# Kernel tuning notes

Hardware: AMD Instinct MI355X
Metric: run time of the kernel (lower is better)

Reference implementation:

```python
import jax, jax.numpy as jnp
import numpy as np

H = 256  # hidden dim, hard-coded in the torch module
DROP_P = 0.25


def setup_inputs() -> dict:
    key = jax.random.key(0)
    ks = jax.random.split(key, 8)
    B, T, D, C = 512, 512, 128, 1000
    x = jax.random.normal(ks[0], (B, T, D), dtype=jnp.float32)
    W_ih = jax.random.normal(ks[1], (3 * H, D), dtype=jnp.float32) * (1.0 / np.sqrt(H))
    W_hh = jax.random.normal(ks[2], (3 * H, H), dtype=jnp.float32) * (1.0 / np.sqrt(H))
    b_ih = jax.random.normal(ks[3], (3 * H,), dtype=jnp.float32) * 0.01
    b_hh = jax.random.normal(ks[4], (3 * H,), dtype=jnp.float32) * 0.01
    W_out = jax.random.normal(ks[5], (C, H), dtype=jnp.float32) * (1.0 / np.sqrt(H))
    b_out = jax.random.normal(ks[6], (C,), dtype=jnp.float32) * 0.01
    # inverted dropout masks per timestep: [T, B, H]
    keep = jax.random.bernoulli(ks[7], 1.0 - DROP_P, (T, B, H))
    drop_mask = keep.astype(jnp.float32) / (1.0 - DROP_P)
    return {"x": x, "W_ih": W_ih, "W_hh": W_hh, "b_ih": b_ih, "b_hh": b_hh,
            "W_out": W_out, "b_out": b_out, "drop_mask": drop_mask}


def _gru_scan(x_tbd, drop_mask, W_ih, W_hh, b_ih, b_hh):
    B = x_tbd.shape[1]
    h0 = jnp.zeros((B, H), dtype=x_tbd.dtype)

    def step(h, inp):
        x_t, m_t = inp
        gi = x_t @ W_ih.T + b_ih        # [B, 3H]
        gh = h @ W_hh.T + b_hh          # [B, 3H]
        i_r, i_z, i_n = gi[:, :H], gi[:, H:2 * H], gi[:, 2 * H:]
        h_r, h_z, h_n = gh[:, :H], gh[:, H:2 * H], gh[:, 2 * H:]
        r = jax.nn.sigmoid(i_r + h_r)
        z = jax.nn.sigmoid(i_z + h_z)
        n = jnp.tanh(i_n + r * h_n)
        h_new = (1.0 - z) * n + z * h
        h_new = h_new * m_t             # dropout per timestep
        return h_new, None

    h_final, _ = jax.lax.scan(step, h0, (x_tbd, drop_mask))
    return h_final


def reference(x, W_ih, W_hh, b_ih, b_hh, W_out, b_out, drop_mask):
    # x: [B, T, D] -> time-major [T, B, D] for scan
    x_tbd = jnp.transpose(x, (1, 0, 2))
    h = _gru_scan(x_tbd, drop_mask, W_ih, W_hh, b_ih, b_hh)
    return h @ W_out.T + b_out          # [B, num_classes]
```

## Files before the change

kernel.cpp:

```cpp
#include <hip/hip_runtime.h>
#include <stdint.h>

#define T_STEPS 512
#define BATCH   512
#define DIN     128
#define HID     256
#define NCLS    1000

typedef unsigned int u32;
typedef unsigned long long u64;
typedef __attribute__((ext_vector_type(8))) short  short8;
typedef __attribute__((ext_vector_type(4))) short  short4v;
typedef __attribute__((ext_vector_type(4))) float  f32x4;

__device__ __forceinline__ short f2bf(float f){
  u32 u = __float_as_uint(f);
  u32 r = (u + 0x7FFFu + ((u >> 16) & 1u)) >> 16;
  return (short)r;
}
__device__ __forceinline__ float bf2f(unsigned short s){
  return __uint_as_float(((u32)s) << 16);
}
__device__ __forceinline__ short8 cvt8(f32x4 a, f32x4 b){
  short8 v;
  v[0]=f2bf(a[0]); v[1]=f2bf(a[1]); v[2]=f2bf(a[2]); v[3]=f2bf(a[3]);
  v[4]=f2bf(b[0]); v[5]=f2bf(b[1]); v[6]=f2bf(b[2]); v[7]=f2bf(b[3]);
  return v;
}
__device__ __forceinline__ void gload_lds16(const void* g, void* l){
  __builtin_amdgcn_global_load_lds(
      (const __attribute__((address_space(1))) unsigned int*)g,
      (__attribute__((address_space(3))) unsigned int*)l, 16, 0, 0);
}

__global__ __launch_bounds__(256) void pack_weights(
    const float* __restrict__ Wih, const float* __restrict__ Whh,
    short* __restrict__ PIH, short* __restrict__ PHH)
{
  int idx = blockIdx.x * 256 + threadIdx.x;
  if (idx >= 48*768) return;
  const float* src; short* dst;
  if (idx < 16*768){
    int kb = idx / 768, j = idx - kb*768;
    src = Wih + (size_t)j*DIN + kb*8;
    dst = PIH + (size_t)idx*8;
  } else {
    int i2 = idx - 16*768;
    int kb = i2 / 768, j = i2 - kb*768;
    src = Whh + (size_t)j*HID + kb*8;
    dst = PHH + (size_t)i2*8;
  }
  short8 v;
  #pragma unroll
  for (int e=0;e<8;e++) v[e] = f2bf(src[e]);
  *(short8*)dst = v;
}

__global__ __launch_bounds__(256) void mask_bits(
    const float* __restrict__ mask, unsigned char* __restrict__ MBo)
{
  int idx = blockIdx.x*256 + threadIdx.x;
  int t = idx >> 14, rem = idx & 16383, bb = rem >> 5, ub = rem & 31;
  const float* mp = mask + ((size_t)t*BATCH + bb)*HID + ub*8;
  u32 byte = 0;
  #pragma unroll
  for (int e=0;e<8;e++) byte |= (mp[e] > 0.5f ? 1u : 0u) << e;
  MBo[((size_t)t*64 + (bb>>3))*256 + (bb&7)*32 + ub] = (unsigned char)byte;
}

__global__ __launch_bounds__(512, 1) void gi_gemm(
    const float* __restrict__ x, const float* __restrict__ b_ih,
    const float* __restrict__ b_hh, const short* __restrict__ PIH,
    short* __restrict__ GIbf, float* __restrict__ GIn)
{
  __shared__ __align__(16) short XT[64*136];
  const int tid = threadIdx.x;
  const int gb  = blockIdx.x >> 6;
  const int tc  = blockIdx.x & 63;
  const int tp0 = tc*4;
  const int w = tid>>6, l = tid&63, c = l&15, g4 = l>>4;

  short8 bfr[6][4]; float bj[6];
  #pragma unroll
  for (int q=0;q<6;q++){
    const int j = (w*6+q)*16 + c;
    #pragma unroll
    for (int kt=0;kt<4;kt++)
      bfr[q][kt] = *(const short8*)(PIH + ((size_t)(kt*4+g4)*768 + j)*8);
    bj[q] = b_ih[j] + (j < 512 ? b_hh[j] : 0.f);
  }

  {
    const int row = tid>>3, cc = (tid&7)*16;
    const int r = row&7, tpl = row>>4, tt = (row>>3)&1;
    const int bb = gb*8 + r;
    const int t  = (tp0+tpl)*2 + tt;
    const float* src = x + ((size_t)bb*T_STEPS + t)*DIN + cc;
    f32x4 a0 = *(const f32x4*)src,     a1 = *(const f32x4*)(src+4);
    f32x4 a2 = *(const f32x4*)(src+8), a3 = *(const f32x4*)(src+12);
    *(short8*)&XT[row*136 + cc]     = cvt8(a0,a1);
    *(short8*)&XT[row*136 + cc + 8] = cvt8(a2,a3);
  }
  __syncthreads();

  const f32x4 z4 = {0.f,0.f,0.f,0.f};
  #pragma unroll
  for (int mt=0; mt<4; ++mt){
    f32x4 acc[6];
    #pragma unroll
    for (int q=0;q<6;q++) acc[q] = z4;
    #pragma unroll
    for (int kt=0;kt<4;kt++){
      short8 af = *(const short8*)&XT[(mt*16+c)*136 + kt*32 + g4*8];
      #pragma unroll
      for (int q=0;q<6;q++)
        acc[q] = __builtin_amdgcn_mfma_f32_16x16x32_bf16(af, bfr[q][kt], acc[q], 0,0,0);
    }
    const int tp = tp0 + mt;
    const size_t base16 = ((size_t)gb*256 + tp)*16;
    #pragma unroll
    for (int q=0;q<6;q++){
      const int j = (w*6+q)*16 + c;
      if (j < 512){
        #pragma unroll
        for (int i=0;i<4;i++)
          GIbf[(base16 + g4*4+i)*512 + j] = f2bf(acc[q][i] + bj[q]);
      } else {
        #pragma unroll
        for (int i=0;i<4;i++)
          GIn[(base16 + g4*4+i)*256 + (j-512)] = acc[q][i] + bj[q];
      }
    }
  }
}

__global__ __launch_bounds__(512, 1) void gru_scan(
    const float* __restrict__ b_hh, const unsigned char* __restrict__ MB,
    const short* __restrict__ PHH, const short* __restrict__ GIbf,
    const float* __restrict__ GIn, float* __restrict__ HFIN)
{
  __shared__ __align__(16) short Ah[16*264];
  __shared__ __align__(16) float Gs[8*776];
  __shared__ __align__(16) short GiRZ[2][8*512];
  __shared__ __align__(16) float GiN [2][8*256];

  const int tid = threadIdx.x;
  const int gb  = blockIdx.x;
  const int w = tid>>6, l = tid&63, c = l&15, g4 = l>>4;

  short8 whf[6][8];
  #pragma unroll
  for (int q=0;q<6;q++){
    const int j = (w*6+q)*16 + c;
    #pragma unroll
    for (int kt=0;kt<8;kt++)
      whf[q][kt] = *(const short8*)(PHH + ((size_t)(kt*4+g4)*768 + j)*8);
  }

  const int b  = tid>>6;
  const int u4 = (tid&63)*4;
  const f32x4 bhn4 = *(const f32x4*)(b_hh + 512 + u4);
  const int mboff = b*32 + ((tid&63)>>1);
  const int mshift = ((tid&63)&1) << 2;

  for (int i=tid; i<16*264; i+=512) Ah[i] = 0;

  const char* srz = (const char*)GIbf + (size_t)gb*256*16*512*2;
  const char* sn  = (const char*)GIn  + (size_t)gb*256*16*256*4;

  {
    gload_lds16(srz + (size_t)0*8192 + w*1024 + l*16, (char*)&GiRZ[0][w*512]);
    gload_lds16(sn  + (size_t)0*8192 + w*1024 + l*16, (char*)&GiN [0][w*256]);
  }
  u32 mbcur = MB[(size_t)gb*256 + mboff];
  float hreg[4] = {0.f,0.f,0.f,0.f};
  asm volatile("s_waitcnt vmcnt(0)" ::: "memory");
  __syncthreads();

  const int ar_off = c*264;
  const f32x4 z4 = {0.f,0.f,0.f,0.f};

  for (int t=0; t<T_STEPS; ++t){
    const int buf = t & 1;
    u32 mbnext = 0;
    if (t < T_STEPS-1){
      gload_lds16(srz + (size_t)(t+1)*8192 + w*1024 + l*16, (char*)&GiRZ[buf^1][w*512]);
      gload_lds16(sn  + (size_t)(t+1)*8192 + w*1024 + l*16, (char*)&GiN [buf^1][w*256]);
      mbnext = MB[((size_t)(t+1)*64 + gb)*256 + mboff];
    }
    f32x4 acc[6];
    #pragma unroll
    for (int q=0;q<6;q++) acc[q] = z4;
    #pragma unroll
    for (int kt=0;kt<8;kt++){
      short8 af = *(const short8*)&Ah[ar_off + kt*32 + g4*8];
      #pragma unroll
      for (int q=0;q<6;q++)
        acc[q] = __builtin_amdgcn_mfma_f32_16x16x32_bf16(af, whf[q][kt], acc[q], 0,0,0);
    }
    if (g4 < 2){
      #pragma unroll
      for (int q=0;q<6;q++){
        const int j = (w*6+q)*16 + c;
        #pragma unroll
        for (int i=0;i<4;i++)
          Gs[(g4*4+i)*776 + j] = acc[q][i];
      }
    }
    asm volatile("s_waitcnt lgkmcnt(0)" ::: "memory");
    __builtin_amdgcn_sched_barrier(0);
    __builtin_amdgcn_s_barrier();
    __builtin_amdgcn_sched_barrier(0);
    {
      f32x4 gr = *(const f32x4*)&Gs[b*776       + u4];
      f32x4 gz = *(const f32x4*)&Gs[b*776 + 256 + u4];
      f32x4 gn = *(const f32x4*)&Gs[b*776 + 512 + u4];
      short4v sr = *(const short4v*)&GiRZ[buf][b*512       + u4];
      short4v sz = *(const short4v*)&GiRZ[buf][b*512 + 256 + u4];
      f32x4 gin = *(const f32x4*)&GiN[buf][b*256 + u4];
      short hb0,hb1,hb2,hb3;
      #pragma unroll
      for (int e=0;e<4;e++){
        float r_ = 1.f/(1.f + __expf(-(gr[e] + bf2f((unsigned short)sr[e]))));
        float z_ = 1.f/(1.f + __expf(-(gz[e] + bf2f((unsigned short)sz[e]))));
        float e2 = __expf(2.f*(gin[e] + r_*(gn[e] + bhn4[e])));
        float n_ = 1.f - 2.f/(e2 + 1.f);
        float mv = ((mbcur >> (mshift + e)) & 1u) ? 1.3333334f : 0.f;
        hreg[e] = ((1.f - z_)*n_ + z_*hreg[e]) * mv;
      }
      hb0=f2bf(hreg[0]); hb1=f2bf(hreg[1]); hb2=f2bf(hreg[2]); hb3=f2bf(hreg[3]);
      short4v hv; hv[0]=hb0; hv[1]=hb1; hv[2]=hb2; hv[3]=hb3;
      *(short4v*)&Ah[b*264 + u4] = hv;
    }
    mbcur = mbnext;
    asm volatile("s_waitcnt vmcnt(0)" ::: "memory");
    __syncthreads();
  }

  f32x4 hv; hv[0]=hreg[0]; hv[1]=hreg[1]; hv[2]=hreg[2]; hv[3]=hreg[3];
  *(f32x4*)&HFIN[((size_t)(gb*8 + b))*HID + u4] = hv;
}

__global__ __launch_bounds__(256) void out_gemm(
    const float* __restrict__ Hf, const float* __restrict__ Wout,
    const float* __restrict__ bout, float* __restrict__ out)
{
  __shared__ __align__(16) float hl[16*256];
  const int bb0 = (blockIdx.x >> 4) * 16;
  const int cc0 = (blockIdx.x & 15) * 64;
  for (int i=threadIdx.x; i<16*256; i+=256) hl[i] = Hf[(size_t)bb0*HID + i];
  __syncthreads();
  const int cc = cc0 + (threadIdx.x & 63);
  const int br = threadIdx.x >> 6;
  if (cc >= NCLS) return;
  const f32x4* wr = (const f32x4*)(Wout + (size_t)cc*HID);
  float a0=0.f, a1=0.f, a2=0.f, a3=0.f;
  #pragma unroll 8
  for (int k4=0;k4<64;k4++){
    f32x4 wv = wr[k4];
    #pragma unroll
    for (int e=0;e<4;e++){
      float we = wv[e]; int k = k4*4+e;
      a0 += hl[(br   )*256+k]*we;
      a1 += hl[(br+ 4)*256+k]*we;
      a2 += hl[(br+ 8)*256+k]*we;
      a3 += hl[(br+12)*256+k]*we;
    }
  }
  float bo = bout[cc];
  out[(size_t)(bb0+br   )*NCLS + cc] = a0 + bo;
  out[(size_t)(bb0+br+ 4)*NCLS + cc] = a1 + bo;
  out[(size_t)(bb0+br+ 8)*NCLS + cc] = a2 + bo;
  out[(size_t)(bb0+br+12)*NCLS + cc] = a3 + bo;
}

extern "C" void kernel_launch(void* const* d_in, const int* in_sizes, int n_in,
                              void* d_out, int out_size, void* d_ws, size_t ws_size,
                              hipStream_t stream) {
  const float* x     = (const float*)d_in[0];
  const float* W_ih  = (const float*)d_in[1];
  const float* W_hh  = (const float*)d_in[2];
  const float* b_ih  = (const float*)d_in[3];
  const float* b_hh  = (const float*)d_in[4];
  const float* W_out = (const float*)d_in[5];
  const float* b_out = (const float*)d_in[6];
  const float* dmask = (const float*)d_in[7];

  if (ws_size < 546373632ull) return;
  short* PIH  = (short*)d_ws;
  short* PHH  = (short*)((char*)d_ws + 196608);
  float* HFIN = (float*)((char*)d_ws + 589824);
  unsigned char* MBp = (unsigned char*)d_ws + 1114112;
  short* GIbf = (short*)((char*)d_ws + 9502720);
  float* GIn  = (float*)((char*)d_ws + 277938176);

  pack_weights<<<144, 256, 0, stream>>>(W_ih, W_hh, PIH, PHH);
  mask_bits<<<32768, 256, 0, stream>>>(dmask, MBp);
  gi_gemm<<<4096, 512, 0, stream>>>(x, b_ih, b_hh, PIH, GIbf, GIn);
  gru_scan<<<64, 512, 0, stream>>>(b_hh, MBp, PHH, GIbf, GIn, HFIN);
  out_gemm<<<512, 256, 0, stream>>>(HFIN, W_out, b_out, (float*)d_out);
}
```

Measured before the change: 1.787 ms.

## Stage GI outputs through LDS for coalesced stores; register-prefetch scan inputs

The input-projection GEMM now writes its results into shared-memory tiles and then stores them to global memory as contiguous 16-byte vectors, replacing scattered 2- and 4-byte stores. The recurrent scan drops the asynchronous global-to-LDS double buffer and instead prefetches the next timestep's gate inputs and mask bits into registers. Each step copies these into a single LDS buffer, and the loop is unrolled by two so the register buffers alternate. Launch bounds for the scan are raised to allow two blocks per CU. In exchange the scan adds a second barrier per step and higher register pressure, which could cause spills.

```diff
diff --git a/kernel.cpp b/kernel.cpp
--- a/kernel.cpp
+++ b/kernel.cpp
@@ -26,11 +26,6 @@
   v[0]=f2bf(a[0]); v[1]=f2bf(a[1]); v[2]=f2bf(a[2]); v[3]=f2bf(a[3]);
   v[4]=f2bf(b[0]); v[5]=f2bf(b[1]); v[6]=f2bf(b[2]); v[7]=f2bf(b[3]);
   return v;
-}
-__device__ __forceinline__ void gload_lds16(const void* g, void* l){
-  __builtin_amdgcn_global_load_lds(
-      (const __attribute__((address_space(1))) unsigned int*)g,
-      (__attribute__((address_space(3))) unsigned int*)l, 16, 0, 0);
 }
 
 __global__ __launch_bounds__(256) void pack_weights(
@@ -74,6 +69,8 @@
     short* __restrict__ GIbf, float* __restrict__ GIn)
 {
   __shared__ __align__(16) short XT[64*136];
+  __shared__ __align__(16) short ORZ[16*520];
+  __shared__ __align__(16) float ON [16*264];
   const int tid = threadIdx.x;
   const int gb  = blockIdx.x >> 6;
   const int tc  = blockIdx.x & 63;
@@ -104,7 +101,7 @@
   __syncthreads();
 
   const f32x4 z4 = {0.f,0.f,0.f,0.f};
-  #pragma unroll
+  #pragma unroll 1
   for (int mt=0; mt<4; ++mt){
     f32x4 acc[6];
     #pragma unroll
@@ -116,33 +113,55 @@
       for (int q=0;q<6;q++)
         acc[q] = __builtin_amdgcn_mfma_f32_16x16x32_bf16(af, bfr[q][kt], acc[q], 0,0,0);
     }
-    const int tp = tp0 + mt;
-    const size_t base16 = ((size_t)gb*256 + tp)*16;
     #pragma unroll
     for (int q=0;q<6;q++){
       const int j = (w*6+q)*16 + c;
-      if (j < 512){
-        #pragma unroll
-        for (int i=0;i<4;i++)
-          GIbf[(base16 + g4*4+i)*512 + j] = f2bf(acc[q][i] + bj[q]);
-      } else {
-        #pragma unroll
-        for (int i=0;i<4;i++)
-          GIn[(base16 + g4*4+i)*256 + (j-512)] = acc[q][i] + bj[q];
+      #pragma unroll
+      for (int i=0;i<4;i++){
+        const int r16 = g4*4+i;
+        const float v = acc[q][i] + bj[q];
+        if (j < 512) ORZ[r16*520 + j] = f2bf(v);
+        else         ON [r16*264 + (j-512)] = v;
       }
     }
-  }
-}
-
-__global__ __launch_bounds__(512, 1) void gru_scan(
+    __syncthreads();
+    {
+      const size_t gbase = (size_t)gb*2097152;
+      #pragma unroll
+      for (int pass=0; pass<2; ++pass){
+        const int chunk = pass*512 + tid;
+        const int tt  = chunk >> 9;
+        const int rem = chunk & 511;
+        const int row = rem >> 6, c16 = rem & 63;
+        short8 vv = *(const short8*)&ORZ[(tt*8+row)*520 + c16*8];
+        const int t = (tp0+mt)*2 + tt;
+        *(short8*)(GIbf + gbase + (size_t)t*4096 + rem*8) = vv;
+      }
+      const size_t nbase = (size_t)gb*1048576;
+      #pragma unroll
+      for (int pass=0; pass<2; ++pass){
+        const int chunk = pass*512 + tid;
+        const int tt  = chunk >> 9;
+        const int rem = chunk & 511;
+        const int row = rem >> 6, c4 = rem & 63;
+        f32x4 vv = *(const f32x4*)&ON[(tt*8+row)*264 + c4*4];
+        const int t = (tp0+mt)*2 + tt;
+        *(f32x4*)(GIn + nbase + (size_t)t*2048 + rem*4) = vv;
+      }
+    }
+    __syncthreads();
+  }
+}
+
+__global__ __launch_bounds__(512, 2) void gru_scan(
     const float* __restrict__ b_hh, const unsigned char* __restrict__ MB,
     const short* __restrict__ PHH, const short* __restrict__ GIbf,
     const float* __restrict__ GIn, float* __restrict__ HFIN)
 {
   __shared__ __align__(16) short Ah[16*264];
   __shared__ __align__(16) float Gs[8*776];
-  __shared__ __align__(16) short GiRZ[2][8*512];
-  __shared__ __align__(16) float GiN [2][8*256];
+  __shared__ __align__(16) short GiRZs[8*512];
+  __shared__ __align__(16) float GiNs [8*256];
 
   const int tid = threadIdx.x;
   const int gb  = blockIdx.x;
@@ -165,77 +184,85 @@
 
   for (int i=tid; i<16*264; i+=512) Ah[i] = 0;
 
-  const char* srz = (const char*)GIbf + (size_t)gb*256*16*512*2;
-  const char* sn  = (const char*)GIn  + (size_t)gb*256*16*256*4;
-
-  {
-    gload_lds16(srz + (size_t)0*8192 + w*1024 + l*16, (char*)&GiRZ[0][w*512]);
-    gload_lds16(sn  + (size_t)0*8192 + w*1024 + l*16, (char*)&GiN [0][w*256]);
-  }
-  u32 mbcur = MB[(size_t)gb*256 + mboff];
+  const char* srz = (const char*)GIbf + (size_t)gb*4194304;
+  const char* sn  = (const char*)GIn  + (size_t)gb*4194304;
+  const int gioff = w*1024 + l*16;
+  const int ar_off = c*264;
+  const int gbase = (g4*4)*776 + w*96 + c;
+
+  asm volatile("" ::: "memory");
+
+  short8 rzA = *(const short8*)(srz + gioff);
+  f32x4  nA  = *(const f32x4 *)(sn  + gioff);
+  u32    mkA = MB[(size_t)gb*256 + mboff];
+  short8 rzB; f32x4 nB; u32 mkB;
   float hreg[4] = {0.f,0.f,0.f,0.f};
-  asm volatile("s_waitcnt vmcnt(0)" ::: "memory");
   __syncthreads();
 
-  const int ar_off = c*264;
   const f32x4 z4 = {0.f,0.f,0.f,0.f};
 
-  for (int t=0; t<T_STEPS; ++t){
-    const int buf = t & 1;
-    u32 mbnext = 0;
-    if (t < T_STEPS-1){
-      gload_lds16(srz + (size_t)(t+1)*8192 + w*1024 + l*16, (char*)&GiRZ[buf^1][w*512]);
-      gload_lds16(sn  + (size_t)(t+1)*8192 + w*1024 + l*16, (char*)&GiN [buf^1][w*256]);
-      mbnext = MB[((size_t)(t+1)*64 + gb)*256 + mboff];
-    }
-    f32x4 acc[6];
-    #pragma unroll
-    for (int q=0;q<6;q++) acc[q] = z4;
-    #pragma unroll
-    for (int kt=0;kt<8;kt++){
-      short8 af = *(const short8*)&Ah[ar_off + kt*32 + g4*8];
-      #pragma unroll
-      for (int q=0;q<6;q++)
-        acc[q] = __builtin_amdgcn_mfma_f32_16x16x32_bf16(af, whf[q][kt], acc[q], 0,0,0);
-    }
-    if (g4 < 2){
-      #pragma unroll
-      for (int q=0;q<6;q++){
-        const int j = (w*6+q)*16 + c;
-        #pragma unroll
-        for (int i=0;i<4;i++)
-          Gs[(g4*4+i)*776 + j] = acc[q][i];
-      }
-    }
-    asm volatile("s_waitcnt lgkmcnt(0)" ::: "memory");
-    __builtin_amdgcn_sched_barrier(0);
-    __builtin_amdgcn_s_barrier();
-    __builtin_amdgcn_sched_barrier(0);
-    {
-      f32x4 gr = *(const f32x4*)&Gs[b*776       + u4];
-      f32x4 gz = *(const f32x4*)&Gs[b*776 + 256 + u4];
-      f32x4 gn = *(const f32x4*)&Gs[b*776 + 512 + u4];
-      short4v sr = *(const short4v*)&GiRZ[buf][b*512       + u4];
-      short4v sz = *(const short4v*)&GiRZ[buf][b*512 + 256 + u4];
-      f32x4 gin = *(const f32x4*)&GiN[buf][b*256 + u4];
-      short hb0,hb1,hb2,hb3;
-      #pragma unroll
-      for (int e=0;e<4;e++){
-        float r_ = 1.f/(1.f + __expf(-(gr[e] + bf2f((unsigned short)sr[e]))));
-        float z_ = 1.f/(1.f + __expf(-(gz[e] + bf2f((unsigned short)sz[e]))));
-        float e2 = __expf(2.f*(gin[e] + r_*(gn[e] + bhn4[e])));
-        float n_ = 1.f - 2.f/(e2 + 1.f);
-        float mv = ((mbcur >> (mshift + e)) & 1u) ? 1.3333334f : 0.f;
-        hreg[e] = ((1.f - z_)*n_ + z_*hreg[e]) * mv;
-      }
-      hb0=f2bf(hreg[0]); hb1=f2bf(hreg[1]); hb2=f2bf(hreg[2]); hb3=f2bf(hreg[3]);
-      short4v hv; hv[0]=hb0; hv[1]=hb1; hv[2]=hb2; hv[3]=hb3;
-      *(short4v*)&Ah[b*264 + u4] = hv;
-    }
-    mbcur = mbnext;
-    asm volatile("s_waitcnt vmcnt(0)" ::: "memory");
-    __syncthreads();
-  }
+#define STEP(T, RZC, NC, MC, RZN, NN, MN) {                                    \
+  const int tn = ((T) < T_STEPS-1) ? (T)+1 : (T);                              \
+                          \
+  *(short8*)&GiRZs[w*512 + l*8] = RZC;                                         \
+  *(f32x4 *)&GiNs [w*256 + l*4] = NC;                                          \
+              \
+  RZN = *(const short8*)(srz + (size_t)tn*8192 + gioff);                       \
+  NN  = *(const f32x4 *)(sn  + (size_t)tn*8192 + gioff);                      \
+  MN  = MB[((size_t)tn*64 + gb)*256 + mboff];                                  \
+                                      \
+  f32x4 acc[6];                                                                \
+  _Pragma("unroll") for (int q=0;q<6;q++) acc[q] = z4;                         \
+  _Pragma("unroll") for (int kt=0;kt<8;kt++){                                  \
+    short8 af = *(const short8*)&Ah[ar_off + kt*32 + g4*8];                    \
+    _Pragma("unroll") for (int q=0;q<6;q++)                                    \
+      acc[q] = __builtin_amdgcn_mfma_f32_16x16x32_bf16(af, whf[q][kt], acc[q], 0,0,0); \
+  }                                                                            \
+                              \
+  if (g4 < 2){                                                                 \
+    _Pragma("unroll") for (int q=0;q<6;q++){                                   \
+      _Pragma("unroll") for (int i=0;i<4;i++)                                  \
+        Gs[gbase + i*776 + q*16] = acc[q][i];                                  \
+    }                                                                          \
+  }                                                                            \
+                          \
+  asm volatile("s_waitcnt lgkmcnt(0)" ::: "memory");                           \
+  __builtin_amdgcn_sched_barrier(0);                                           \
+  __builtin_amdgcn_s_barrier();                                                \
+  __builtin_amdgcn_sched_barrier(0);                                           \
+                                                                 \
+  {                                                                            \
+    f32x4 gr = *(const f32x4*)&Gs[b*776       + u4];                           \
+    f32x4 gz = *(const f32x4*)&Gs[b*776 + 256 + u4];                           \
+    f32x4 gn = *(const f32x4*)&Gs[b*776 + 512 + u4];                           \
+    short4v sr = *(const short4v*)&GiRZs[b*512       + u4];                    \
+    short4v sz = *(const short4v*)&GiRZs[b*512 + 256 + u4];                    \
+    f32x4 gin = *(const f32x4*)&GiNs[b*256 + u4];                              \
+    _Pragma("unroll") for (int e=0;e<4;e++){                                   \
+      float r_ = 1.f/(1.f + __expf(-(gr[e] + bf2f((unsigned short)sr[e]))));   \
+      float z_ = 1.f/(1.f + __expf(-(gz[e] + bf2f((unsigned short)sz[e]))));   \
+      float e2 = __expf(2.f*(gin[e] + r_*(gn[e] + bhn4[e])));                  \
+      float n_ = 1.f - 2.f/(e2 + 1.f);                                         \
+      float mv = ((MC >> (mshift + e)) & 1u) ? 1.3333334f : 0.f;               \
+      hreg[e] = ((1.f - z_)*n_ + z_*hreg[e]) * mv;                             \
+    }                                                                          \
+    short4v hv;                                                                \
+    hv[0]=f2bf(hreg[0]); hv[1]=f2bf(hreg[1]);                                  \
+    hv[2]=f2bf(hreg[2]); hv[3]=f2bf(hreg[3]);                                  \
+    *(short4v*)&Ah[b*264 + u4] = hv;                                           \
+  }                                                                            \
+                                                \
+  asm volatile("s_waitcnt lgkmcnt(0)" ::: "memory");                           \
+  __builtin_amdgcn_sched_barrier(0);                                           \
+  __builtin_amdgcn_s_barrier();                                                \
+  __builtin_amdgcn_sched_barrier(0);                                           \
+}
+
+  for (int t2=0; t2<T_STEPS; t2+=2){
+    STEP(t2,   rzA, nA, mkA, rzB, nB, mkB);
+    STEP(t2+1, rzB, nB, mkB, rzA, nA, mkA);
+  }
+#undef STEP
 
   f32x4 hv; hv[0]=hreg[0]; hv[1]=hreg[1]; hv[2]=hreg[2]; hv[3]=hreg[3];
   *(f32x4*)&HFIN[((size_t)(gb*8 + b))*HID + u4] = hv;
```

After: 2.365 ms. +32.3%, slower.
